# Kernel optimization log

Measured on AMD Instinct MI355X. Metric: run time of the kernel, lower is better.

## Reference

```python
import jax, jax.numpy as jnp
import numpy as np

GAMMA = 0.99
EPS = 1e-8
N = 16777216  # flattened reward count


def setup_inputs() -> dict:
    key = jax.random.key(0)
    rewards = jax.random.normal(key, (N,), dtype=jnp.float32)
    return {"rewards": rewards}


def reference(rewards):
    # Sequential recurrence: R_t = gamma*R_{t-1} + r_t, Welford stats over R_t,
    # scaled[i] = r_i / max(std_t, eps), std_t = sqrt(var_sum/count) (1.0 if count < 2).
    flat = rewards.reshape(-1)

    def step(carry, r):
        R, cnt, mean, var_sum = carry
        R = GAMMA * R + r
        cnt = cnt + 1.0
        delta = R - mean
        mean = mean + delta / cnt
        var_sum = var_sum + delta * (R - mean)
        std = jnp.where(cnt < 2.0, jnp.float32(1.0), jnp.sqrt(var_sum / cnt))
        std = jnp.maximum(std, jnp.float32(EPS))
        return (R, cnt, mean, var_sum), r / std

    init = (jnp.float32(0.0), jnp.float32(0.0), jnp.float32(0.0), jnp.float32(0.0))
    _, scaled = jax.lax.scan(step, init, flat)
    return scaled.reshape(rewards.shape)
```

## Files before the change

kernel.cpp:

```cpp
#include <hip/hip_runtime.h>
#include <math.h>

#define THREADS 256
#define GAMMA 0.99

template<int LPT>
__device__ __forceinline__ int padi(int i) { return i + (i >> LPT); }

template<int NW>
__device__ __forceinline__ void block_compose_excl(int tid, double g, double v,
                                                   double& eg, double& ev,
                                                   double* lg, double* lv) {
    const int lane = tid & 63, wave = tid >> 6;
    double ig = g, iv = v;
#pragma unroll
    for (int k = 1; k < 64; k <<= 1) {
        double og = __shfl_up(ig, k);
        double ov = __shfl_up(iv, k);
        if (lane >= k) { iv = fma(ig, ov, iv); ig *= og; }
    }
    double weg = __shfl_up(ig, 1);
    double wev = __shfl_up(iv, 1);
    if (lane == 0) { weg = 1.0; wev = 0.0; }
    if (lane == 63) { lg[wave] = ig; lv[wave] = iv; }
    __syncthreads();
    double bg = 1.0, bv = 0.0;
    for (int w = 0; w < wave; ++w) { bv = fma(lg[w], bv, lv[w]); bg *= lg[w]; }
    eg = weg * bg;
    ev = fma(weg, bv, wev);
}

template<int NW>
__device__ __forceinline__ void block_add_excl2(int tid, double a, double b,
                                                double& ea, double& eb,
                                                double* la, double* lb) {
    const int lane = tid & 63, wave = tid >> 6;
    double ia = a, ib = b;
#pragma unroll
    for (int k = 1; k < 64; k <<= 1) {
        double oa = __shfl_up(ia, k);
        double ob = __shfl_up(ib, k);
        if (lane >= k) { ia += oa; ib += ob; }
    }
    double wea = __shfl_up(ia, 1);
    double web = __shfl_up(ib, 1);
    if (lane == 0) { wea = 0.0; web = 0.0; }
    if (lane == 63) { la[wave] = ia; lb[wave] = ib; }
    __syncthreads();
    double ba = 0.0, bb = 0.0;
    for (int w = 0; w < wave; ++w) { ba += la[w]; bb += lb[w]; }
    ea = wea + ba;
    eb = web + bb;
}

template<int PT, int LPT>
__global__ __launch_bounds__(THREADS) void rs_phase1(const float* __restrict__ in,
                                                     double* __restrict__ ws, int nchunk) {
    constexpr int CHUNKE = THREADS * PT;
    __shared__ double lg[4], lv[4], r1[4], r2[4], r3[4];
    const int tid = threadIdx.x, lane = tid & 63, wave = tid >> 6;
    const int chunk = blockIdx.x;
    const float* src = in + (size_t)chunk * CHUNKE + (size_t)tid * PT;

    float rv[PT];
#pragma unroll
    for (int q = 0; q < PT / 4; ++q) {
        const float4 t = ((const float4*)src)[q];
        rv[4 * q] = t.x; rv[4 * q + 1] = t.y; rv[4 * q + 2] = t.z; rv[4 * q + 3] = t.w;
    }
    const float gf = (float)GAMMA;
    float p = 0.f, psum = 0.f, pq = 0.f, p2 = 0.f, gp = 1.f;
#pragma unroll
    for (int j = 0; j < PT; ++j) {
        p = fmaf(gf, p, rv[j]);
        gp *= gf;
        psum += p;
        pq = fmaf(gp, p, pq);
        p2 = fmaf(p, p, p2);
    }
    const double g = GAMMA;
    double gPT = g;
#pragma unroll
    for (int e = 0; e < LPT; ++e) gPT *= gPT;

    double eg, ev;
    block_compose_excl<4>(tid, gPT, (double)p, eg, ev, lg, lv);
    const double rho = ev, gexc = eg;

    const double G1 = g * (1.0 - gPT) / (1.0 - g);
    const double G2 = g * g * (1.0 - gPT * gPT) / (1.0 - g * g);
    double c1 = fma(rho, G1, (double)psum);
    double c2 = gexc * fma(rho, G2, (double)pq);
    double c3 = fma(rho * rho, G2, fma(2.0 * rho, (double)pq, (double)p2));
#pragma unroll
    for (int k = 32; k > 0; k >>= 1) {
        c1 += __shfl_down(c1, k);
        c2 += __shfl_down(c2, k);
        c3 += __shfl_down(c3, k);
    }
    if (lane == 0) { r1[wave] = c1; r2[wave] = c2; r3[wave] = c3; }
    __syncthreads();
    if (tid == 0) {
        double A = 0.0;
#pragma unroll
        for (int w = 0; w < 4; ++w) A = fma(lg[w], A, lv[w]);
        ws[chunk]              = A;
        ws[nchunk + chunk]     = r1[0] + r1[1] + r1[2] + r1[3];
        ws[2 * nchunk + chunk] = r2[0] + r2[1] + r2[2] + r2[3];
        ws[3 * nchunk + chunk] = r3[0] + r3[1] + r3[2] + r3[3];
    }
}

template<int CPT, int LOG2CHUNK>
__global__ __launch_bounds__(1024) void rs_phase2(double* __restrict__ ws, int nchunk) {
    __shared__ double lg[16], lv[16], la[16], lb[16];
    const int t = threadIdx.x;
    const double g = GAMMA;
    double gC = g;
#pragma unroll
    for (int e = 0; e < LOG2CHUNK; ++e) gC *= gC;

    double A[CPT], Ps[CPT], Pq[CPT], P2[CPT];
    const int c0 = t * CPT;
#pragma unroll
    for (int i = 0; i < CPT; ++i) {
        const int c = c0 + i;
        const bool ok = c < nchunk;
        A[i]  = ok ? ws[c] : 0.0;
        Ps[i] = ok ? ws[nchunk + c] : 0.0;
        Pq[i] = ok ? ws[2 * nchunk + c] : 0.0;
        P2[i] = ok ? ws[3 * nchunk + c] : 0.0;
    }
    double mg = 1.0, mv = 0.0;
#pragma unroll
    for (int i = 0; i < CPT; ++i) { mv = fma(gC, mv, A[i]); mg *= gC; }

    double eg, ev;
    block_compose_excl<16>(t, mg, mv, eg, ev, lg, lv);

    const double G1C = g * (1.0 - gC) / (1.0 - g);
    const double G2C = g * g * (1.0 - gC * gC) / (1.0 - g * g);
    double Rin[CPT + 1];
    Rin[0] = ev;
    double s1[CPT], s2[CPT];
#pragma unroll
    for (int i = 0; i < CPT; ++i) {
        s1[i] = fma(Rin[i], G1C, Ps[i]);
        s2[i] = fma(Rin[i] * Rin[i], G2C, fma(2.0 * Rin[i], Pq[i], P2[i]));
        Rin[i + 1] = fma(gC, Rin[i], A[i]);
    }
    double ts1 = 0.0, ts2 = 0.0;
#pragma unroll
    for (int i = 0; i < CPT; ++i) { ts1 += s1[i]; ts2 += s2[i]; }
    double ea, eb;
    block_add_excl2<16>(t, ts1, ts2, ea, eb, la, lb);
#pragma unroll
    for (int i = 0; i < CPT; ++i) {
        const int c = c0 + i;
        if (c < nchunk) {
            ws[4 * nchunk + c] = Rin[i];
            ws[5 * nchunk + c] = ea;
            ws[6 * nchunk + c] = eb;
        }
        ea += s1[i];
        eb += s2[i];
    }
}

template<int PT, int LPT>
__global__ __launch_bounds__(THREADS) void rs_phase3(const float* __restrict__ in,
                                                     float* __restrict__ out,
                                                     const double* __restrict__ ws, int nchunk) {
    constexpr int CHUNKE = THREADS * PT;
    __shared__ float sbuf[CHUNKE + THREADS];
    __shared__ double lg[4], lv[4], la[4], lb[4];
    const int tid = threadIdx.x;
    const int chunk = blockIdx.x;
    const float* src = in + (size_t)chunk * CHUNKE + (size_t)tid * PT;

    float rv[PT];
#pragma unroll
    for (int q = 0; q < PT / 4; ++q) {
        const float4 t = ((const float4*)src)[q];
        rv[4 * q] = t.x; rv[4 * q + 1] = t.y; rv[4 * q + 2] = t.z; rv[4 * q + 3] = t.w;
    }
    const float gf = (float)GAMMA;
    float p = 0.f, psum = 0.f, pq = 0.f, p2 = 0.f, gp = 1.f;
#pragma unroll
    for (int j = 0; j < PT; ++j) {
        p = fmaf(gf, p, rv[j]);
        gp *= gf;
        psum += p;
        pq = fmaf(gp, p, pq);
        p2 = fmaf(p, p, p2);
    }
    const double g = GAMMA;
    double gPT = g;
#pragma unroll
    for (int e = 0; e < LPT; ++e) gPT *= gPT;

    double eg, ev;
    block_compose_excl<4>(tid, gPT, (double)p, eg, ev, lg, lv);

    const double RinC = ws[4 * nchunk + chunk];
    const double S1C  = ws[5 * nchunk + chunk];
    const double S2C  = ws[6 * nchunk + chunk];
    const double rin  = fma(eg, RinC, ev);

    const double G1 = g * (1.0 - gPT) / (1.0 - g);
    const double G2 = g * g * (1.0 - gPT * gPT) / (1.0 - g * g);
    const double s1 = fma(rin, G1, (double)psum);
    const double s2 = fma(rin * rin, G2, fma(2.0 * rin, (double)pq, (double)p2));
    double ea, eb;
    block_add_excl2<4>(tid, s1, s2, ea, eb, la, lb);
    const double S1b = S1C + ea;
    const double S2b = S2C + eb;

    const int a0 = padi<LPT>(tid * PT);

    if (chunk == 0) {
        double R = rin, S1 = S1b, S2 = S2b;
        const size_t gbase = (size_t)tid * PT;
        for (int j = 0; j < PT; ++j) {
            const float rf = rv[j];
            R = fma(g, R, (double)rf);
            S1 += R;
            S2 = fma(R, R, S2);
            float ov;
            if (gbase + j == 0) {
                ov = rf;
            } else {
                const double cnt = (double)(gbase + j + 1);
                const double inv = 1.0 / cnt;
                const double mean = S1 * inv;
                double var = fma(S2, inv, -(mean * mean));
                var = var > 0.0 ? var : 0.0;
                double sd = sqrt(var);
                sd = sd > 1e-8 ? sd : 1e-8;
                ov = (float)((double)rf / sd);
            }
            sbuf[a0 + j] = ov;
        }
    } else {
        float R = (float)rin;
        float ls1 = 0.f, ls2 = 0.f;
        const float S1bf = (float)S1b, S2bf = (float)S2b;
        const float base_cnt = (float)((size_t)chunk * CHUNKE + (size_t)tid * PT);
#pragma unroll
        for (int j = 0; j < PT; ++j) {
            const float rf = rv[j];
            R = fmaf(gf, R, rf);
            ls1 += R;
            ls2 = fmaf(R, R, ls2);
            const float cnt = base_cnt + (float)(j + 1);
            const float inv = 1.0f / cnt;
            const float S1f = S1bf + ls1;
            const float S2f = S2bf + ls2;
            const float mean = S1f * inv;
            float var = fmaf(S2f, inv, -(mean * mean));
            var = var > 0.f ? var : 0.f;
            float sd = sqrtf(var);
            sd = sd > 1e-8f ? sd : 1e-8f;
            sbuf[a0 + j] = rf / sd;
        }
    }
    __syncthreads();

    float* dst = out + (size_t)chunk * CHUNKE;
    for (int i = tid * 4; i < CHUNKE; i += THREADS * 4) {
        const int pp = padi<LPT>(i);
        *(float4*)(dst + i) = make_float4(sbuf[pp], sbuf[pp + 1], sbuf[pp + 2], sbuf[pp + 3]);
    }
}

extern "C" void kernel_launch(void* const* d_in, const int* in_sizes, int n_in,
                              void* d_out, int out_size, void* d_ws, size_t ws_size,
                              hipStream_t stream) {
    (void)n_in; (void)out_size;
    const float* in = (const float*)d_in[0];
    float* out = (float*)d_out;
    double* ws = (double*)d_ws;
    const int n = in_sizes[0];

    const int nc16 = n / 4096;
    if ((n % 4096) == 0 && nc16 >= 1 && nc16 <= 4096 &&
        ws_size >= (size_t)7 * (size_t)nc16 * sizeof(double)) {
        rs_phase1<16, 4><<<nc16, THREADS, 0, stream>>>(in, ws, nc16);
        rs_phase2<4, 12><<<1, 1024, 0, stream>>>(ws, nc16);
        rs_phase3<16, 4><<<nc16, THREADS, 0, stream>>>(in, out, ws, nc16);
    } else {
        const int nc64 = n / 16384;
        rs_phase1<64, 6><<<nc64, THREADS, 0, stream>>>(in, ws, nc64);
        rs_phase2<1, 14><<<1, 1024, 0, stream>>>(ws, nc64);
        rs_phase3<64, 6><<<nc64, THREADS, 0, stream>>>(in, out, ws, nc64);
    }
}
```

Before: 57.27 us.

## Interleave chunk aggregates, simplify per-element std math, use nontemporal stores

Stores the per-chunk aggregates and carries interleaved as an array of structs rather than separate planes. In the phase-3 inner loop, the divide, sqrt and divide are replaced by a single hardware reciprocal square root on the unnormalised variance. Output writes become nontemporal vector stores to reduce cache pollution. The fallback path's phase2 template argument also changes. The rsq approximation and the clamp at 1e-12 can alter rounding and edge behaviour compared with the exact sqrt and divide.

```diff
diff --git a/kernel.cpp b/kernel.cpp
--- a/kernel.cpp
+++ b/kernel.cpp
@@ -3,6 +3,8 @@
 
 #define THREADS 256
 #define GAMMA 0.99
+
+typedef float vf4 __attribute__((ext_vector_type(4)));
 
 template<int LPT>
 __device__ __forceinline__ int padi(int i) { return i + (i >> LPT); }
@@ -55,7 +57,7 @@
 
 template<int PT, int LPT>
 __global__ __launch_bounds__(THREADS) void rs_phase1(const float* __restrict__ in,
-                                                     double* __restrict__ ws, int nchunk) {
+                                                     double* __restrict__ agg, int nchunk) {
     constexpr int CHUNKE = THREADS * PT;
     __shared__ double lg[4], lv[4], r1[4], r2[4], r3[4];
     const int tid = threadIdx.x, lane = tid & 63, wave = tid >> 6;
@@ -104,15 +106,16 @@
         double A = 0.0;
 #pragma unroll
         for (int w = 0; w < 4; ++w) A = fma(lg[w], A, lv[w]);
-        ws[chunk]              = A;
-        ws[nchunk + chunk]     = r1[0] + r1[1] + r1[2] + r1[3];
-        ws[2 * nchunk + chunk] = r2[0] + r2[1] + r2[2] + r2[3];
-        ws[3 * nchunk + chunk] = r3[0] + r3[1] + r3[2] + r3[3];
+        agg[4 * (size_t)chunk + 0] = A;
+        agg[4 * (size_t)chunk + 1] = r1[0] + r1[1] + r1[2] + r1[3];
+        agg[4 * (size_t)chunk + 2] = r2[0] + r2[1] + r2[2] + r2[3];
+        agg[4 * (size_t)chunk + 3] = r3[0] + r3[1] + r3[2] + r3[3];
     }
 }
 
 template<int CPT, int LOG2CHUNK>
-__global__ __launch_bounds__(1024) void rs_phase2(double* __restrict__ ws, int nchunk) {
+__global__ __launch_bounds__(1024) void rs_phase2(const double* __restrict__ agg,
+                                                  double* __restrict__ car, int nchunk) {
     __shared__ double lg[16], lv[16], la[16], lb[16];
     const int t = threadIdx.x;
     const double g = GAMMA;
@@ -126,10 +129,10 @@
     for (int i = 0; i < CPT; ++i) {
         const int c = c0 + i;
         const bool ok = c < nchunk;
-        A[i]  = ok ? ws[c] : 0.0;
-        Ps[i] = ok ? ws[nchunk + c] : 0.0;
-        Pq[i] = ok ? ws[2 * nchunk + c] : 0.0;
-        P2[i] = ok ? ws[3 * nchunk + c] : 0.0;
+        A[i]  = ok ? agg[4 * (size_t)c + 0] : 0.0;
+        Ps[i] = ok ? agg[4 * (size_t)c + 1] : 0.0;
+        Pq[i] = ok ? agg[4 * (size_t)c + 2] : 0.0;
+        P2[i] = ok ? agg[4 * (size_t)c + 3] : 0.0;
     }
     double mg = 1.0, mv = 0.0;
 #pragma unroll
@@ -158,9 +161,9 @@
     for (int i = 0; i < CPT; ++i) {
         const int c = c0 + i;
         if (c < nchunk) {
-            ws[4 * nchunk + c] = Rin[i];
-            ws[5 * nchunk + c] = ea;
-            ws[6 * nchunk + c] = eb;
+            car[3 * (size_t)c + 0] = Rin[i];
+            car[3 * (size_t)c + 1] = ea;
+            car[3 * (size_t)c + 2] = eb;
         }
         ea += s1[i];
         eb += s2[i];
@@ -170,7 +173,7 @@
 template<int PT, int LPT>
 __global__ __launch_bounds__(THREADS) void rs_phase3(const float* __restrict__ in,
                                                      float* __restrict__ out,
-                                                     const double* __restrict__ ws, int nchunk) {
+                                                     const double* __restrict__ car, int nchunk) {
     constexpr int CHUNKE = THREADS * PT;
     __shared__ float sbuf[CHUNKE + THREADS];
     __shared__ double lg[4], lv[4], la[4], lb[4];
@@ -202,9 +205,9 @@
     double eg, ev;
     block_compose_excl<4>(tid, gPT, (double)p, eg, ev, lg, lv);
 
-    const double RinC = ws[4 * nchunk + chunk];
-    const double S1C  = ws[5 * nchunk + chunk];
-    const double S2C  = ws[6 * nchunk + chunk];
+    const double RinC = car[3 * (size_t)chunk + 0];
+    const double S1C  = car[3 * (size_t)chunk + 1];
+    const double S2C  = car[3 * (size_t)chunk + 2];
     const double rin  = fma(eg, RinC, ev);
 
     const double G1 = g * (1.0 - gPT) / (1.0 - g);
@@ -253,15 +256,11 @@
             ls1 += R;
             ls2 = fmaf(R, R, ls2);
             const float cnt = base_cnt + (float)(j + 1);
-            const float inv = 1.0f / cnt;
             const float S1f = S1bf + ls1;
             const float S2f = S2bf + ls2;
-            const float mean = S1f * inv;
-            float var = fmaf(S2f, inv, -(mean * mean));
-            var = var > 0.f ? var : 0.f;
-            float sd = sqrtf(var);
-            sd = sd > 1e-8f ? sd : 1e-8f;
-            sbuf[a0 + j] = rf / sd;
+            float t = fmaf(S2f, cnt, -(S1f * S1f));
+            t = fmaxf(t, 1e-12f);
+            sbuf[a0 + j] = rf * cnt * __builtin_amdgcn_rsqf(t);
         }
     }
     __syncthreads();
@@ -269,7 +268,9 @@
     float* dst = out + (size_t)chunk * CHUNKE;
     for (int i = tid * 4; i < CHUNKE; i += THREADS * 4) {
         const int pp = padi<LPT>(i);
-        *(float4*)(dst + i) = make_float4(sbuf[pp], sbuf[pp + 1], sbuf[pp + 2], sbuf[pp + 3]);
+        vf4 v;
+        v.x = sbuf[pp]; v.y = sbuf[pp + 1]; v.z = sbuf[pp + 2]; v.w = sbuf[pp + 3];
+        __builtin_nontemporal_store(v, (vf4*)(dst + i));
     }
 }
 
@@ -282,16 +283,20 @@
     double* ws = (double*)d_ws;
     const int n = in_sizes[0];
 
-    const int nc16 = n / 4096;
-    if ((n % 4096) == 0 && nc16 >= 1 && nc16 <= 4096 &&
-        ws_size >= (size_t)7 * (size_t)nc16 * sizeof(double)) {
-        rs_phase1<16, 4><<<nc16, THREADS, 0, stream>>>(in, ws, nc16);
-        rs_phase2<4, 12><<<1, 1024, 0, stream>>>(ws, nc16);
-        rs_phase3<16, 4><<<nc16, THREADS, 0, stream>>>(in, out, ws, nc16);
+    const int nc = n / 4096;
+    if ((n % 4096) == 0 && nc >= 1 && nc <= 4096 &&
+        ws_size >= (size_t)7 * nc * sizeof(double)) {
+        double* agg = ws;
+        double* car = ws + 4 * (size_t)nc;
+        rs_phase1<16, 4><<<nc, THREADS, 0, stream>>>(in, agg, nc);
+        rs_phase2<4, 12><<<1, 1024, 0, stream>>>(agg, car, nc);
+        rs_phase3<16, 4><<<nc, THREADS, 0, stream>>>(in, out, car, nc);
     } else {
         const int nc64 = n / 16384;
-        rs_phase1<64, 6><<<nc64, THREADS, 0, stream>>>(in, ws, nc64);
-        rs_phase2<1, 14><<<1, 1024, 0, stream>>>(ws, nc64);
-        rs_phase3<64, 6><<<nc64, THREADS, 0, stream>>>(in, out, ws, nc64);
-    }
-}
+        double* agg = ws;
+        double* car = ws + 4 * (size_t)nc64;
+        rs_phase1<64, 6><<<nc64, THREADS, 0, stream>>>(in, agg, nc64);
+        rs_phase2<4, 14><<<1, 1024, 0, stream>>>(agg, car, nc64);
+        rs_phase3<64, 6><<<nc64, THREADS, 0, stream>>>(in, out, car, nc64);
+    }
+}
```

Result: faster. 55.02 us (-3.9%).
